# Performance work log

Hardware: AMD Instinct MI355X
Metric: run time of the kernel (lower is better)

The kernel has to match this reference:

```python
import jax, jax.numpy as jnp
import numpy as np

B, L1, L2 = 16, 32, 128
DEC = 512       # decoder_size
MEM = 512       # memory_bank_size
TOP = 50        # topic_num


def setup_inputs() -> dict:
    key = jax.random.key(0)
    ks = jax.random.split(key, 16)
    s = lambda fan_in: 1.0 / np.sqrt(fan_in)
    inp = {
        "decoder_state": jax.random.normal(ks[0], (B, DEC), jnp.float32),
        "doc_memory": jax.random.normal(ks[1], (B, L1, MEM), jnp.float32),
        "word_memory": jax.random.normal(ks[2], (B, L1, L2, MEM), jnp.float32),
        "topic_dist": jax.random.uniform(ks[3], (B, TOP), jnp.float32),
        "doc_mask": jnp.ones((B, L1), jnp.int32),
        "word_mask": jnp.ones((B, L1, L2), jnp.int32),
        # HierAttention params (PyTorch Linear weight layout: [out, in])
        "Wv": jax.random.uniform(ks[4], (1, DEC), jnp.float32, -s(DEC), s(DEC)),
        "Wd": jax.random.uniform(ks[5], (DEC, DEC), jnp.float32, -s(DEC), s(DEC)),
        "Wt": jax.random.uniform(ks[6], (DEC, TOP), jnp.float32, -s(TOP), s(TOP)),
        "Wm": jax.random.uniform(ks[7], (DEC, MEM), jnp.float32, -s(MEM), s(MEM)),
        # doc_attention (inner Attention) params
        "Wv2": jax.random.uniform(ks[8], (1, DEC), jnp.float32, -s(DEC), s(DEC)),
        "Wd2": jax.random.uniform(ks[9], (DEC, DEC), jnp.float32, -s(DEC), s(DEC)),
        "Wt2": jax.random.uniform(ks[10], (DEC, TOP), jnp.float32, -s(TOP), s(TOP)),
        "Wm2": jax.random.uniform(ks[11], (DEC, MEM), jnp.float32, -s(MEM), s(MEM)),
    }
    return inp


def reference(decoder_state, doc_memory, word_memory, topic_dist,
              doc_mask, word_mask,
              Wv, Wd, Wt, Wm, Wv2, Wd2, Wt2, Wm2):
    neg_inf = jnp.float32(-jnp.inf)

    # ---- word-level (HierAttention.score) ----
    enc_feat = jnp.einsum('bqwm,dm->bqwd', word_memory, Wm)      # [B,L1,L2,DEC]
    dec_feat = decoder_state @ Wd.T                              # [B,DEC]
    top_feat = topic_dist @ Wt.T                                 # [B,DEC]
    e = jnp.tanh(enc_feat + (dec_feat + top_feat)[:, None, None, :])
    word_scores = jnp.einsum('bqwd,od->bqw', e, Wv)[..., 0] if Wv.shape[0] != 1 else jnp.einsum('bqwd,d->bqw', e, Wv[0])
    word_scores = jnp.where(word_mask == 0, neg_inf, word_scores)
    word_attn = jax.nn.softmax(word_scores, axis=-1)             # [B,L1,L2]

    # ---- doc-level (Attention.score) ----
    enc_feat_d = jnp.einsum('bqm,dm->bqd', doc_memory, Wm2)      # [B,L1,DEC]
    dec_feat_d = decoder_state @ Wd2.T                           # [B,DEC]
    top_feat_d = topic_dist @ Wt2.T                              # [B,DEC]
    e_d = jnp.tanh(enc_feat_d + (dec_feat_d + top_feat_d)[:, None, :])
    doc_scores = jnp.einsum('bqd,d->bq', e_d, Wv2[0])            # [B,L1]
    doc_scores = jnp.where(doc_mask == 0, neg_inf, doc_scores)
    doc_attn = jax.nn.softmax(doc_scores, axis=-1)               # [B,L1]

    # ---- combine ----
    rescaled = doc_attn[..., None] * word_attn                   # [B,L1,L2]
    context = jnp.einsum('bqw,bqwm->bm', rescaled, word_memory)  # [B,MEM]
    return context, rescaled
```

## Files before the change

kernel.cpp:

```cpp
#include <hip/hip_runtime.h>
#include <hip/hip_bf16.h>
#include <math.h>

#define BATCH 16
#define L1 32
#define L2 128
#define DEC 512
#define MEM 512
#define TOPN 50
#define NROWS (BATCH * L1 * L2)
#define NBQ (BATCH * L1)

typedef short short8 __attribute__((ext_vector_type(8)));
typedef float f32x16 __attribute__((ext_vector_type(16)));

#define WS_WP     0
#define WS_WP2    131072
#define WS_BIAS1  262144
#define WS_BIAS2  270336
#define WS_DOCSC  278528

__device__ __forceinline__ unsigned int pkbf(float a, float b) {
    __hip_bfloat162 h = __float22bfloat162_rn(float2{a, b});
    union { __hip_bfloat162 h; unsigned int u; } c{h};
    return c.u;
}

__device__ __forceinline__ float fast_tanh(float x) {
    return 1.f - 2.f / (__expf(2.f * x) + 1.f);
}

__global__ __launch_bounds__(256) void setup_kernel(
    const float* __restrict__ Wm, const float* __restrict__ Wm2,
    unsigned short* __restrict__ Wp, unsigned short* __restrict__ Wp2,
    const float* __restrict__ dec, const float* __restrict__ topic,
    const float* __restrict__ Wd, const float* __restrict__ Wt,
    const float* __restrict__ Wd2, const float* __restrict__ Wt2,
    float* __restrict__ bias1, float* __restrict__ bias2,
    float* __restrict__ ctx_out)
{
    const int bid = blockIdx.x;
    const int tid = threadIdx.x;
    if (bid < 128) {
        int s = bid * 256 + tid;
        int C = s >> 10;
        int u = s & 1023;
        int nt = u >> 6, k8 = (u >> 5) & 1, n_in = u & 31;
        int d = nt * 32 + n_in;
        int k = C * 16 + k8 * 8;

        const float4* src = (const float4*)(Wm + (size_t)d * DEC + k);
        float4 v0 = src[0], v1 = src[1];
        uint4 v;
        v.x = pkbf(v0.x, v0.y); v.y = pkbf(v0.z, v0.w);
        v.z = pkbf(v1.x, v1.y); v.w = pkbf(v1.z, v1.w);
        ((uint4*)Wp)[s] = v;

        const float4* src2 = (const float4*)(Wm2 + (size_t)d * DEC + k);
        float4 w0 = src2[0], w1 = src2[1];
        uint4 w;
        w.x = pkbf(w0.x, w0.y); w.y = pkbf(w0.z, w0.w);
        w.z = pkbf(w1.x, w1.y); w.w = pkbf(w1.z, w1.w);
        ((uint4*)Wp2)[s] = w;
    } else if (bid < 128 + 4096) {
        int gw = (bid - 128) * 4 + (tid >> 6);
        int lane = tid & 63;
        int mat = gw >> 13;
        int rem = gw & 8191;
        int bb = rem >> 9;
        int d = rem & 511;

        const float* wrow = (mat ? Wd2 : Wd) + (size_t)d * DEC;
        const float* drow = dec + (size_t)bb * DEC;
        float4 a0 = ((const float4*)wrow)[lane * 2];
        float4 a1 = ((const float4*)wrow)[lane * 2 + 1];
        float4 x0 = ((const float4*)drow)[lane * 2];
        float4 x1 = ((const float4*)drow)[lane * 2 + 1];
        float acc = a0.x * x0.x;
        acc = fmaf(a0.y, x0.y, acc);
        acc = fmaf(a0.z, x0.z, acc);
        acc = fmaf(a0.w, x0.w, acc);
        acc = fmaf(a1.x, x1.x, acc);
        acc = fmaf(a1.y, x1.y, acc);
        acc = fmaf(a1.z, x1.z, acc);
        acc = fmaf(a1.w, x1.w, acc);
        const float* trow = (mat ? Wt2 : Wt) + (size_t)d * TOPN;
        if (lane < TOPN) acc = fmaf(trow[lane], topic[bb * TOPN + lane], acc);
#pragma unroll
        for (int o = 1; o <= 32; o <<= 1) acc += __shfl_xor(acc, o);
        if (lane == 0) (mat ? bias2 : bias1)[bb * DEC + d] = acc;
    } else {
        int i = (bid - (128 + 4096)) * 256 + tid;
        float4 z = {0.f, 0.f, 0.f, 0.f};
        ((float4*)ctx_out)[i * 2] = z;
        ((float4*)ctx_out)[i * 2 + 1] = z;
    }
}

__global__ __launch_bounds__(512, 2) void score_fused_kernel(
    const float* __restrict__ X,
    const unsigned short* __restrict__ Wp_,
    const float* __restrict__ Wv_,
    const float* __restrict__ bias_,
    const float* __restrict__ doc_scores,
    const int* __restrict__ doc_mask,
    const int* __restrict__ word_mask,
    float* __restrict__ rescaled_out,
    float* __restrict__ ctx_out,
    float* __restrict__ scores_out,
    int mode)
{
    __shared__ __align__(16) char lsA[128 * 1040];
    __shared__ float red[8][128];
    __shared__ float sS[128];
    __shared__ float rmax2[2], rsum2[2];
    __shared__ float s_dattn;
    __shared__ __align__(16) float4 part[3 * 128];

    const int tid = threadIdx.x;
    const int lane = tid & 63;
    const int w = tid >> 6;
    const int bid = blockIdx.x;
    const int r0 = bid * 128;
    const int col = lane & 31;
    const int h = lane >> 5;

    const int q0 = bid & 3;
    const int Q[4] = { q0, (q0 + 1) & 3, (q0 + 2) & 3, (q0 + 3) & 3 };
#define CH_AT(f) (Q[(f) >> 3] * 8 + ((f) & 7))

    const int scol = tid & 31;
    const int srow0 = tid >> 5;
    const float4* Xbase = (const float4*)X + (size_t)(r0 + srow0) * 128 + scol;
    char* const wbase = lsA + (size_t)srow0 * 1040 + scol * 8;

#define ISSUEQ(buf, qq) { _Pragma("unroll") for (int i = 0; i < 8; ++i) \
        buf[i] = Xbase[(size_t)(16 * i) * 128 + (qq) * 32]; }
#define WRITEQ(buf, qq) { _Pragma("unroll") for (int i = 0; i < 8; ++i) { \
        uint2 ww; ww.x = pkbf(buf[i].x, buf[i].y); ww.y = pkbf(buf[i].z, buf[i].w); \
        *(uint2*)(wbase + (size_t)(16 * i) * 1040 + (qq) * 256) = ww; } }
#define LGKMBAR { asm volatile("s_waitcnt lgkmcnt(0)" ::: "memory"); \
                  __builtin_amdgcn_s_barrier(); asm volatile("" ::: "memory"); }
#define MFMA(a, bb, c) __builtin_amdgcn_mfma_f32_32x32x16_bf16(a, bb, c, 0, 0, 0)

    const uint4* Bq4 = (const uint4*)Wp_;
    const int vB = w * 128 + lane;

    const char* const aR0 = lsA + (size_t)col * 1040 + h * 16;
    const char* const aR1 = aR0 + 32 * 1040;
    const char* const aR2 = aR0 + 64 * 1040;
    const char* const aR3 = aR0 + 96 * 1040;

    f32x16 acc[8];
#pragma unroll
    for (int t = 0; t < 8; ++t)
        acc[t] = (f32x16){0.f,0.f,0.f,0.f, 0.f,0.f,0.f,0.f, 0.f,0.f,0.f,0.f, 0.f,0.f,0.f,0.f};

    uint4 rb[4][2];

#define STEP(f, a0q, a1q, a2q, a3q) { \
        union { uint4 u; short8 s8; } b0{rb[(f) & 3][0]}, b1{rb[(f) & 3][1]}; \
        if ((f) + 4 < 32) { \
            const int cn_ = CH_AT((f) + 4); \
            rb[(f) & 3][0] = Bq4[(size_t)cn_ * 1024 + vB]; \
            rb[(f) & 3][1] = Bq4[(size_t)cn_ * 1024 + vB + 64]; \
        } \
        short8 a0 = *(const short8*)((a0q) + ((f) & 7) * 32); \
        short8 a1 = *(const short8*)((a1q) + ((f) & 7) * 32); \
        short8 a2 = *(const short8*)((a2q) + ((f) & 7) * 32); \
        short8 a3 = *(const short8*)((a3q) + ((f) & 7) * 32); \
        acc[0] = MFMA(a0, b0.s8, acc[0]); \
        acc[1] = MFMA(a0, b1.s8, acc[1]); \
        acc[2] = MFMA(a1, b0.s8, acc[2]); \
        acc[3] = MFMA(a1, b1.s8, acc[3]); \
        acc[4] = MFMA(a2, b0.s8, acc[4]); \
        acc[5] = MFMA(a2, b1.s8, acc[5]); \
        acc[6] = MFMA(a3, b0.s8, acc[6]); \
        acc[7] = MFMA(a3, b1.s8, acc[7]); }

#define QUARTER(j, f0) { \
        const int qo_ = Q[j] * 256; \
        const char* a0q = aR0 + qo_; const char* a1q = aR1 + qo_; \
        const char* a2q = aR2 + qo_; const char* a3q = aR3 + qo_; \
        STEP((f0) + 0, a0q, a1q, a2q, a3q) STEP((f0) + 1, a0q, a1q, a2q, a3q) \
        STEP((f0) + 2, a0q, a1q, a2q, a3q) STEP((f0) + 3, a0q, a1q, a2q, a3q) \
        STEP((f0) + 4, a0q, a1q, a2q, a3q) STEP((f0) + 5, a0q, a1q, a2q, a3q) \
        STEP((f0) + 6, a0q, a1q, a2q, a3q) STEP((f0) + 7, a0q, a1q, a2q, a3q) }

    float4 sb0[8], sb1[8];
    ISSUEQ(sb0, Q[0]);
    ISSUEQ(sb1, Q[1]);

    if (mode == 0 && tid < 32) {
        int b_ = bid >> 5;
        int di = b_ * 32 + tid;
        float dsv = doc_scores[di];
        if (doc_mask[di] == 0) dsv = -INFINITY;
        float mx = dsv;
#pragma unroll
        for (int o = 1; o <= 16; o <<= 1) mx = fmaxf(mx, __shfl_xor(mx, o));
        float e = __expf(dsv - mx);
        float sum = e;
#pragma unroll
        for (int o = 1; o <= 16; o <<= 1) sum += __shfl_xor(sum, o);
        if (tid == (bid & 31)) s_dattn = e / sum;
    }

    WRITEQ(sb0, Q[0]);
#pragma unroll
    for (int f = 0; f < 4; ++f) {
        const int c_ = CH_AT(f);
        rb[f][0] = Bq4[(size_t)c_ * 1024 + vB];
        rb[f][1] = Bq4[(size_t)c_ * 1024 + vB + 64];
    }
    LGKMBAR;

    ISSUEQ(sb0, Q[2]);
    QUARTER(0, 0);
    WRITEQ(sb1, Q[1]);
    LGKMBAR;

    ISSUEQ(sb1, Q[3]);
    QUARTER(1, 8);
    WRITEQ(sb0, Q[2]);
    LGKMBAR;

    QUARTER(2, 16);
    WRITEQ(sb1, Q[3]);
    LGKMBAR;

    QUARTER(3, 24);

    {
        const int d0 = w * 64 + col;
        const float wv0 = Wv_[d0], wv1 = Wv_[d0 + 32];
#pragma unroll
        for (int rg = 0; rg < 4; ++rg) {
            const int brg = mode ? (bid * 4 + rg) : (bid >> 5);
            const float bs0 = bias_[brg * DEC + d0];
            const float bs1 = bias_[brg * DEC + d0 + 32];
#pragma unroll
            for (int r = 0; r < 16; ++r) {
                float val = fmaf(wv0, fast_tanh(acc[rg * 2 + 0][r] + bs0),
                                 wv1 * fast_tanh(acc[rg * 2 + 1][r] + bs1));
                val += __shfl_xor(val, 16);
                val += __shfl_xor(val, 8);
                val += __shfl_xor(val, 4);
                val += __shfl_xor(val, 2);
                val += __shfl_xor(val, 1);
                if (col == r) {
                    int row_in = (r & 3) + 8 * (r >> 2) + 4 * h;
                    red[w][rg * 32 + row_in] = val;
                }
            }
        }
    }
    __syncthreads();

    if (mode) {
        if (tid < 128)
            scores_out[r0 + tid] = red[0][tid] + red[1][tid] + red[2][tid] + red[3][tid]
                                 + red[4][tid] + red[5][tid] + red[6][tid] + red[7][tid];
        return;
    }

    float e = 0.f, sv = 0.f;
    if (tid < 128) {
        sv = red[0][tid] + red[1][tid] + red[2][tid] + red[3][tid]
           + red[4][tid] + red[5][tid] + red[6][tid] + red[7][tid];
        if (word_mask[r0 + tid] == 0) sv = -INFINITY;
        float mx = sv;
#pragma unroll
        for (int o = 1; o <= 32; o <<= 1) mx = fmaxf(mx, __shfl_xor(mx, o));
        if (lane == 0) rmax2[w] = mx;
    }
    __syncthreads();
    if (tid < 128) {
        float mx = fmaxf(rmax2[0], rmax2[1]);
        e = __expf(sv - mx);
        float sum = e;
#pragma unroll
        for (int o = 1; o <= 32; o <<= 1) sum += __shfl_xor(sum, o);
        if (lane == 0) rsum2[w] = sum;
    }
    __syncthreads();
    if (tid < 128) {
        float sum = rsum2[0] + rsum2[1];
        float resc = s_dattn * (e / sum);
        sS[tid] = resc;
        rescaled_out[r0 + tid] = resc;
    }
    __syncthreads();

    const int b_ = bid >> 5;
    const int hh = tid >> 7;
    const int m4 = tid & 127;
    const float4* Xr = (const float4*)X + (size_t)r0 * 128 + (size_t)hh * 32 * 128 + m4;
    float4 a = {0.f, 0.f, 0.f, 0.f};
#pragma unroll 8
    for (int i = 0; i < 32; ++i) {
        float rr = sS[hh * 32 + i];
        float4 v = Xr[(size_t)i * 128];
        a.x = fmaf(rr, v.x, a.x);
        a.y = fmaf(rr, v.y, a.y);
        a.z = fmaf(rr, v.z, a.z);
        a.w = fmaf(rr, v.w, a.w);
    }
    if (hh) part[(hh - 1) * 128 + m4] = a;
    __syncthreads();
    if (hh == 0) {
        float4 p0 = part[m4], p1 = part[128 + m4], p2 = part[256 + m4];
        a.x += p0.x + p1.x + p2.x;
        a.y += p0.y + p1.y + p2.y;
        a.z += p0.z + p1.z + p2.z;
        a.w += p0.w + p1.w + p2.w;
        float* dst = ctx_out + (size_t)b_ * MEM + m4 * 4;
        atomicAdd(dst + 0, a.x);
        atomicAdd(dst + 1, a.y);
        atomicAdd(dst + 2, a.z);
        atomicAdd(dst + 3, a.w);
    }
}

extern "C" void kernel_launch(void* const* d_in, const int* in_sizes, int n_in,
                              void* d_out, int out_size, void* d_ws, size_t ws_size,
                              hipStream_t stream) {
    const float* decoder_state = (const float*)d_in[0];
    const float* doc_memory    = (const float*)d_in[1];
    const float* word_memory   = (const float*)d_in[2];
    const float* topic_dist    = (const float*)d_in[3];
    const int*   doc_mask      = (const int*)d_in[4];
    const int*   word_mask     = (const int*)d_in[5];
    const float* Wv  = (const float*)d_in[6];
    const float* Wd  = (const float*)d_in[7];
    const float* Wt  = (const float*)d_in[8];
    const float* Wm  = (const float*)d_in[9];
    const float* Wv2 = (const float*)d_in[10];
    const float* Wd2 = (const float*)d_in[11];
    const float* Wt2 = (const float*)d_in[12];
    const float* Wm2 = (const float*)d_in[13];

    float* ws = (float*)d_ws;
    unsigned short* Wp  = (unsigned short*)(ws + WS_WP);
    unsigned short* Wp2 = (unsigned short*)(ws + WS_WP2);
    float* bias1       = ws + WS_BIAS1;
    float* bias2       = ws + WS_BIAS2;
    float* doc_scores  = ws + WS_DOCSC;

    float* ctx_out      = (float*)d_out;
    float* rescaled_out = (float*)d_out + BATCH * MEM;

    setup_kernel<<<128 + 4096 + 4, 256, 0, stream>>>(Wm, Wm2, Wp, Wp2,
                                                     decoder_state, topic_dist,
                                                     Wd, Wt, Wd2, Wt2, bias1, bias2, ctx_out);
    score_fused_kernel<<<4, 512, 0, stream>>>(doc_memory, Wp2, Wv2, bias2,
                                              nullptr, nullptr, nullptr,
                                              nullptr, nullptr, doc_scores, 1);
    score_fused_kernel<<<NBQ, 512, 0, stream>>>(word_memory, Wp, Wv, bias1,
                                                doc_scores, doc_mask, word_mask,
                                                rescaled_out, ctx_out, nullptr, 0);
}
```

Measured before the change: 315.9 us.

## Split doc scoring into fp32 kernel and widen word kernel to 1024 threads

Replaces the 4-block MFMA doc-score launch with a dedicated 256-block fp32 dot-product kernel reading Wm2 directly, which removes the Wm2 bf16 packing from setup. The word kernel now runs 16 waves per block, each owning 32 output columns with one B fragment, and stages X in double-buffered quarter tiles (2x33KB) instead of one full 130KB tile. The goal is less LDS per block and more waves to hide latency. In exchange, each wave has less MFMA reuse per B load and there are more barriers and partial reductions.

```diff
diff --git a/kernel.cpp b/kernel.cpp
--- a/kernel.cpp
+++ b/kernel.cpp
@@ -30,9 +30,19 @@
     return 1.f - 2.f / (__expf(2.f * x) + 1.f);
 }
 
+__device__ __forceinline__ float wave_sum64(float v) {
+    v += __shfl_xor(v, 1);
+    v += __shfl_xor(v, 2);
+    v += __shfl_xor(v, 4);
+    v += __shfl_xor(v, 8);
+    v += __shfl_xor(v, 16);
+    v += __shfl_xor(v, 32);
+    return v;
+}
+
 __global__ __launch_bounds__(256) void setup_kernel(
-    const float* __restrict__ Wm, const float* __restrict__ Wm2,
-    unsigned short* __restrict__ Wp, unsigned short* __restrict__ Wp2,
+    const float* __restrict__ Wm,
+    unsigned short* __restrict__ Wp,
     const float* __restrict__ dec, const float* __restrict__ topic,
     const float* __restrict__ Wd, const float* __restrict__ Wt,
     const float* __restrict__ Wd2, const float* __restrict__ Wt2,
@@ -55,13 +65,6 @@
         v.x = pkbf(v0.x, v0.y); v.y = pkbf(v0.z, v0.w);
         v.z = pkbf(v1.x, v1.y); v.w = pkbf(v1.z, v1.w);
         ((uint4*)Wp)[s] = v;
-
-        const float4* src2 = (const float4*)(Wm2 + (size_t)d * DEC + k);
-        float4 w0 = src2[0], w1 = src2[1];
-        uint4 w;
-        w.x = pkbf(w0.x, w0.y); w.y = pkbf(w0.z, w0.w);
-        w.z = pkbf(w1.x, w1.y); w.w = pkbf(w1.z, w1.w);
-        ((uint4*)Wp2)[s] = w;
     } else if (bid < 128 + 4096) {
         int gw = (bid - 128) * 4 + (tid >> 6);
         int lane = tid & 63;
@@ -97,7 +100,73 @@
     }
 }
 
-__global__ __launch_bounds__(512, 2) void score_fused_kernel(
+__global__ __launch_bounds__(512) void doc_score_kernel(
+    const float* __restrict__ Xd,
+    const float* __restrict__ Wm2,
+    const float* __restrict__ Wv2,
+    const float* __restrict__ bias2,
+    float* __restrict__ doc_scores)
+{
+    __shared__ float wsum[2][8];
+    const int tid = threadIdx.x;
+    const int lane = tid & 63;
+    const int w = tid >> 6;
+    const int row0 = blockIdx.x * 2;
+    const int b = row0 >> 5;
+
+    const float4* X0 = (const float4*)(Xd + (size_t)row0 * MEM) + lane * 2;
+    const float4* X1 = (const float4*)(Xd + (size_t)(row0 + 1) * MEM) + lane * 2;
+    float4 xa0 = X0[0], xb0 = X0[1];
+    float4 xa1 = X1[0], xb1 = X1[1];
+
+    float s0 = 0.f, s1 = 0.f;
+#pragma unroll 2
+    for (int dd = 0; dd < 64; dd += 2) {
+        const int d = w * 64 + dd;
+        const float4* W0 = (const float4*)(Wm2 + (size_t)d * MEM) + lane * 2;
+        const float4* W1 = (const float4*)(Wm2 + (size_t)(d + 1) * MEM) + lane * 2;
+        float4 wa0 = W0[0], wb0 = W0[1];
+        float4 wa1 = W1[0], wb1 = W1[1];
+
+        float p00 = wa0.x * xa0.x, p01 = wa1.x * xa0.x;
+        float p10 = wa0.x * xa1.x, p11 = wa1.x * xa1.x;
+        p00 = fmaf(wa0.y, xa0.y, p00); p01 = fmaf(wa1.y, xa0.y, p01);
+        p10 = fmaf(wa0.y, xa1.y, p10); p11 = fmaf(wa1.y, xa1.y, p11);
+        p00 = fmaf(wa0.z, xa0.z, p00); p01 = fmaf(wa1.z, xa0.z, p01);
+        p10 = fmaf(wa0.z, xa1.z, p10); p11 = fmaf(wa1.z, xa1.z, p11);
+        p00 = fmaf(wa0.w, xa0.w, p00); p01 = fmaf(wa1.w, xa0.w, p01);
+        p10 = fmaf(wa0.w, xa1.w, p10); p11 = fmaf(wa1.w, xa1.w, p11);
+        p00 = fmaf(wb0.x, xb0.x, p00); p01 = fmaf(wb1.x, xb0.x, p01);
+        p10 = fmaf(wb0.x, xb1.x, p10); p11 = fmaf(wb1.x, xb1.x, p11);
+        p00 = fmaf(wb0.y, xb0.y, p00); p01 = fmaf(wb1.y, xb0.y, p01);
+        p10 = fmaf(wb0.y, xb1.y, p10); p11 = fmaf(wb1.y, xb1.y, p11);
+        p00 = fmaf(wb0.z, xb0.z, p00); p01 = fmaf(wb1.z, xb0.z, p01);
+        p10 = fmaf(wb0.z, xb1.z, p10); p11 = fmaf(wb1.z, xb1.z, p11);
+        p00 = fmaf(wb0.w, xb0.w, p00); p01 = fmaf(wb1.w, xb0.w, p01);
+        p10 = fmaf(wb0.w, xb1.w, p10); p11 = fmaf(wb1.w, xb1.w, p11);
+
+        p00 = wave_sum64(p00);
+        p01 = wave_sum64(p01);
+        p10 = wave_sum64(p10);
+        p11 = wave_sum64(p11);
+        if (lane == 0) {
+            float wva = Wv2[d], wvb = Wv2[d + 1];
+            float bsa = bias2[b * DEC + d], bsb = bias2[b * DEC + d + 1];
+            s0 += fmaf(wva, fast_tanh(p00 + bsa), wvb * fast_tanh(p01 + bsb));
+            s1 += fmaf(wva, fast_tanh(p10 + bsa), wvb * fast_tanh(p11 + bsb));
+        }
+    }
+    if (lane == 0) { wsum[0][w] = s0; wsum[1][w] = s1; }
+    __syncthreads();
+    if (tid < 2) {
+        float s = 0.f;
+#pragma unroll
+        for (int i = 0; i < 8; ++i) s += wsum[tid][i];
+        doc_scores[row0 + tid] = s;
+    }
+}
+
+__global__ __launch_bounds__(1024) void word_fused_kernel(
     const float* __restrict__ X,
     const unsigned short* __restrict__ Wp_,
     const float* __restrict__ Wv_,
@@ -106,16 +175,14 @@
     const int* __restrict__ doc_mask,
     const int* __restrict__ word_mask,
     float* __restrict__ rescaled_out,
-    float* __restrict__ ctx_out,
-    float* __restrict__ scores_out,
-    int mode)
+    float* __restrict__ ctx_out)
 {
-    __shared__ __align__(16) char lsA[128 * 1040];
-    __shared__ float red[8][128];
+    __shared__ __align__(16) char lsQ[2][128 * 264];
+    __shared__ float red[16][128];
     __shared__ float sS[128];
     __shared__ float rmax2[2], rsum2[2];
     __shared__ float s_dattn;
-    __shared__ __align__(16) float4 part[3 * 128];
+    __shared__ __align__(16) float4 part[7 * 128];
 
     const int tid = threadIdx.x;
     const int lane = tid & 63;
@@ -125,73 +192,49 @@
     const int col = lane & 31;
     const int h = lane >> 5;
 
-    const int q0 = bid & 3;
-    const int Q[4] = { q0, (q0 + 1) & 3, (q0 + 2) & 3, (q0 + 3) & 3 };
-#define CH_AT(f) (Q[(f) >> 3] * 8 + ((f) & 7))
-
     const int scol = tid & 31;
     const int srow0 = tid >> 5;
     const float4* Xbase = (const float4*)X + (size_t)(r0 + srow0) * 128 + scol;
-    char* const wbase = lsA + (size_t)srow0 * 1040 + scol * 8;
-
-#define ISSUEQ(buf, qq) { _Pragma("unroll") for (int i = 0; i < 8; ++i) \
-        buf[i] = Xbase[(size_t)(16 * i) * 128 + (qq) * 32]; }
-#define WRITEQ(buf, qq) { _Pragma("unroll") for (int i = 0; i < 8; ++i) { \
-        uint2 ww; ww.x = pkbf(buf[i].x, buf[i].y); ww.y = pkbf(buf[i].z, buf[i].w); \
-        *(uint2*)(wbase + (size_t)(16 * i) * 1040 + (qq) * 256) = ww; } }
+
+    float4 sb[4];
+#define ISSUEQ(qq) { _Pragma("unroll") for (int i = 0; i < 4; ++i) \
+        sb[i] = Xbase[(size_t)(32 * i) * 128 + (qq) * 32]; }
+#define WRITEQ(pb) { char* wp = lsQ[pb] + (size_t)srow0 * 264 + scol * 8; \
+    _Pragma("unroll") for (int i = 0; i < 4; ++i) { \
+        uint2 ww; ww.x = pkbf(sb[i].x, sb[i].y); ww.y = pkbf(sb[i].z, sb[i].w); \
+        *(uint2*)(wp + (size_t)(32 * i) * 264) = ww; } }
 #define LGKMBAR { asm volatile("s_waitcnt lgkmcnt(0)" ::: "memory"); \
                   __builtin_amdgcn_s_barrier(); asm volatile("" ::: "memory"); }
 #define MFMA(a, bb, c) __builtin_amdgcn_mfma_f32_32x32x16_bf16(a, bb, c, 0, 0, 0)
 
     const uint4* Bq4 = (const uint4*)Wp_;
-    const int vB = w * 128 + lane;
-
-    const char* const aR0 = lsA + (size_t)col * 1040 + h * 16;
-    const char* const aR1 = aR0 + 32 * 1040;
-    const char* const aR2 = aR0 + 64 * 1040;
-    const char* const aR3 = aR0 + 96 * 1040;
-
-    f32x16 acc[8];
-#pragma unroll
-    for (int t = 0; t < 8; ++t)
-        acc[t] = (f32x16){0.f,0.f,0.f,0.f, 0.f,0.f,0.f,0.f, 0.f,0.f,0.f,0.f, 0.f,0.f,0.f,0.f};
-
-    uint4 rb[4][2];
-
-#define STEP(f, a0q, a1q, a2q, a3q) { \
-        union { uint4 u; short8 s8; } b0{rb[(f) & 3][0]}, b1{rb[(f) & 3][1]}; \
-        if ((f) + 4 < 32) { \
-            const int cn_ = CH_AT((f) + 4); \
-            rb[(f) & 3][0] = Bq4[(size_t)cn_ * 1024 + vB]; \
-            rb[(f) & 3][1] = Bq4[(size_t)cn_ * 1024 + vB + 64]; \
-        } \
-        short8 a0 = *(const short8*)((a0q) + ((f) & 7) * 32); \
-        short8 a1 = *(const short8*)((a1q) + ((f) & 7) * 32); \
-        short8 a2 = *(const short8*)((a2q) + ((f) & 7) * 32); \
-        short8 a3 = *(const short8*)((a3q) + ((f) & 7) * 32); \
-        acc[0] = MFMA(a0, b0.s8, acc[0]); \
-        acc[1] = MFMA(a0, b1.s8, acc[1]); \
-        acc[2] = MFMA(a1, b0.s8, acc[2]); \
-        acc[3] = MFMA(a1, b1.s8, acc[3]); \
-        acc[4] = MFMA(a2, b0.s8, acc[4]); \
-        acc[5] = MFMA(a2, b1.s8, acc[5]); \
-        acc[6] = MFMA(a3, b0.s8, acc[6]); \
-        acc[7] = MFMA(a3, b1.s8, acc[7]); }
-
-#define QUARTER(j, f0) { \
-        const int qo_ = Q[j] * 256; \
-        const char* a0q = aR0 + qo_; const char* a1q = aR1 + qo_; \
-        const char* a2q = aR2 + qo_; const char* a3q = aR3 + qo_; \
-        STEP((f0) + 0, a0q, a1q, a2q, a3q) STEP((f0) + 1, a0q, a1q, a2q, a3q) \
-        STEP((f0) + 2, a0q, a1q, a2q, a3q) STEP((f0) + 3, a0q, a1q, a2q, a3q) \
-        STEP((f0) + 4, a0q, a1q, a2q, a3q) STEP((f0) + 5, a0q, a1q, a2q, a3q) \
-        STEP((f0) + 6, a0q, a1q, a2q, a3q) STEP((f0) + 7, a0q, a1q, a2q, a3q) }
-
-    float4 sb0[8], sb1[8];
-    ISSUEQ(sb0, Q[0]);
-    ISSUEQ(sb1, Q[1]);
-
-    if (mode == 0 && tid < 32) {
+    const int vB = w * 64 + lane;
+
+    f32x16 acc0, acc1, acc2, acc3;
+    acc0 = acc1 = acc2 = acc3 =
+        (f32x16){0.f,0.f,0.f,0.f, 0.f,0.f,0.f,0.f, 0.f,0.f,0.f,0.f, 0.f,0.f,0.f,0.f};
+
+    uint4 rb[4];
+
+#define STEP(f, pb) { \
+        union { uint4 u; short8 s8; } bb{rb[(f) & 3]}; \
+        if ((f) + 4 < 32) rb[(f) & 3] = Bq4[(size_t)((f) + 4) * 1024 + vB]; \
+        const char* ab = lsQ[pb] + (size_t)col * 264 + h * 16 + ((f) & 7) * 32; \
+        short8 a0 = *(const short8*)(ab); \
+        short8 a1 = *(const short8*)(ab + 32 * 264); \
+        short8 a2 = *(const short8*)(ab + 64 * 264); \
+        short8 a3 = *(const short8*)(ab + 96 * 264); \
+        acc0 = MFMA(a0, bb.s8, acc0); \
+        acc1 = MFMA(a1, bb.s8, acc1); \
+        acc2 = MFMA(a2, bb.s8, acc2); \
+        acc3 = MFMA(a3, bb.s8, acc3); }
+
+#define QUARTER(f0, pb) { STEP((f0)+0, pb) STEP((f0)+1, pb) STEP((f0)+2, pb) STEP((f0)+3, pb) \
+                          STEP((f0)+4, pb) STEP((f0)+5, pb) STEP((f0)+6, pb) STEP((f0)+7, pb) }
+
+    ISSUEQ(0);
+
+    if (tid < 32) {
         int b_ = bid >> 5;
         int di = b_ * 32 + tid;
         float dsv = doc_scores[di];
@@ -206,73 +249,54 @@
         if (tid == (bid & 31)) s_dattn = e / sum;
     }
 
-    WRITEQ(sb0, Q[0]);
-#pragma unroll
-    for (int f = 0; f < 4; ++f) {
-        const int c_ = CH_AT(f);
-        rb[f][0] = Bq4[(size_t)c_ * 1024 + vB];
-        rb[f][1] = Bq4[(size_t)c_ * 1024 + vB + 64];
-    }
+    WRITEQ(0);
+#pragma unroll
+    for (int f = 0; f < 4; ++f) rb[f] = Bq4[(size_t)f * 1024 + vB];
     LGKMBAR;
 
-    ISSUEQ(sb0, Q[2]);
+    ISSUEQ(1);
     QUARTER(0, 0);
-    WRITEQ(sb1, Q[1]);
+    WRITEQ(1);
     LGKMBAR;
 
-    ISSUEQ(sb1, Q[3]);
-    QUARTER(1, 8);
-    WRITEQ(sb0, Q[2]);
+    ISSUEQ(2);
+    QUARTER(8, 1);
+    WRITEQ(0);
     LGKMBAR;
 
-    QUARTER(2, 16);
-    WRITEQ(sb1, Q[3]);
+    ISSUEQ(3);
+    QUARTER(16, 0);
+    WRITEQ(1);
     LGKMBAR;
 
-    QUARTER(3, 24);
+    QUARTER(24, 1);
 
     {
-        const int d0 = w * 64 + col;
-        const float wv0 = Wv_[d0], wv1 = Wv_[d0 + 32];
-#pragma unroll
-        for (int rg = 0; rg < 4; ++rg) {
-            const int brg = mode ? (bid * 4 + rg) : (bid >> 5);
-            const float bs0 = bias_[brg * DEC + d0];
-            const float bs1 = bias_[brg * DEC + d0 + 32];
-#pragma unroll
-            for (int r = 0; r < 16; ++r) {
-                float val = fmaf(wv0, fast_tanh(acc[rg * 2 + 0][r] + bs0),
-                                 wv1 * fast_tanh(acc[rg * 2 + 1][r] + bs1));
-                val += __shfl_xor(val, 16);
-                val += __shfl_xor(val, 8);
-                val += __shfl_xor(val, 4);
-                val += __shfl_xor(val, 2);
-                val += __shfl_xor(val, 1);
-                if (col == r) {
-                    int row_in = (r & 3) + 8 * (r >> 2) + 4 * h;
-                    red[w][rg * 32 + row_in] = val;
-                }
-            }
-        }
-    }
-    __syncthreads();
-
-    if (mode) {
-        if (tid < 128)
-            scores_out[r0 + tid] = red[0][tid] + red[1][tid] + red[2][tid] + red[3][tid]
-                                 + red[4][tid] + red[5][tid] + red[6][tid] + red[7][tid];
-        return;
-    }
+        const int d0 = w * 32 + col;
+        const float wv0 = Wv_[d0];
+        const int bb_ = bid >> 5;
+        const float bs0 = bias_[bb_ * DEC + d0];
+#define EPI(rg, accN) { _Pragma("unroll") for (int r = 0; r < 16; ++r) { \
+            float val = wv0 * fast_tanh(accN[r] + bs0); \
+            val += __shfl_xor(val, 16); val += __shfl_xor(val, 8); \
+            val += __shfl_xor(val, 4);  val += __shfl_xor(val, 2); \
+            val += __shfl_xor(val, 1); \
+            if (col == r) red[w][(rg) * 32 + ((r & 3) + 8 * (r >> 2) + 4 * h)] = val; } }
+        EPI(0, acc0) EPI(1, acc1) EPI(2, acc2) EPI(3, acc3)
+#undef EPI
+    }
+    __syncthreads();
 
     float e = 0.f, sv = 0.f;
     if (tid < 128) {
-        sv = red[0][tid] + red[1][tid] + red[2][tid] + red[3][tid]
-           + red[4][tid] + red[5][tid] + red[6][tid] + red[7][tid];
+        sv = 0.f;
+#pragma unroll
+        for (int i = 0; i < 16; ++i) sv += red[i][tid];
         if (word_mask[r0 + tid] == 0) sv = -INFINITY;
         float mx = sv;
 #pragma unroll
         for (int o = 1; o <= 32; o <<= 1) mx = fmaxf(mx, __shfl_xor(mx, o));
-        if (lane == 0) rmax2[w] = mx;
+        if (lane == 0) rmax2[tid >> 6] = mx;
     }
     __syncthreads();
     if (tid < 128) {
@@ -281,7 +305,7 @@
         float sum = e;
 #pragma unroll
         for (int o = 1; o <= 32; o <<= 1) sum += __shfl_xor(sum, o);
-        if (lane == 0) rsum2[w] = sum;
+        if (lane == 0) rsum2[tid >> 6] = sum;
     }
     __syncthreads();
     if (tid < 128) {
@@ -295,11 +319,11 @@
     const int b_ = bid >> 5;
     const int hh = tid >> 7;
     const int m4 = tid & 127;
-    const float4* Xr = (const float4*)X + (size_t)r0 * 128 + (size_t)hh * 32 * 128 + m4;
+    const float4* Xr = (const float4*)X + (size_t)(r0 + hh * 16) * 128 + m4;
     float4 a = {0.f, 0.f, 0.f, 0.f};
-#pragma unroll 8
-    for (int i = 0; i < 32; ++i) {
-        float rr = sS[hh * 32 + i];
+#pragma unroll 4
+    for (int i = 0; i < 16; ++i) {
+        float rr = sS[hh * 16 + i];
         float4 v = Xr[(size_t)i * 128];
         a.x = fmaf(rr, v.x, a.x);
         a.y = fmaf(rr, v.y, a.y);
@@ -309,11 +333,11 @@
     if (hh) part[(hh - 1) * 128 + m4] = a;
     __syncthreads();
     if (hh == 0) {
-        float4 p0 = part[m4], p1 = part[128 + m4], p2 = part[256 + m4];
-        a.x += p0.x + p1.x + p2.x;
-        a.y += p0.y + p1.y + p2.y;
-        a.z += p0.z + p1.z + p2.z;
-        a.w += p0.w + p1.w + p2.w;
+#pragma unroll
+        for (int p = 0; p < 7; ++p) {
+            float4 pp = part[p * 128 + m4];
+            a.x += pp.x; a.y += pp.y; a.z += pp.z; a.w += pp.w;
+        }
         float* dst = ctx_out + (size_t)b_ * MEM + m4 * 4;
         atomicAdd(dst + 0, a.x);
         atomicAdd(dst + 1, a.y);
@@ -342,7 +366,6 @@
 
     float* ws = (float*)d_ws;
     unsigned short* Wp  = (unsigned short*)(ws + WS_WP);
-    unsigned short* Wp2 = (unsigned short*)(ws + WS_WP2);
     float* bias1       = ws + WS_BIAS1;
     float* bias2       = ws + WS_BIAS2;
     float* doc_scores  = ws + WS_DOCSC;
@@ -350,13 +373,11 @@
     float* ctx_out      = (float*)d_out;
     float* rescaled_out = (float*)d_out + BATCH * MEM;
 
-    setup_kernel<<<128 + 4096 + 4, 256, 0, stream>>>(Wm, Wm2, Wp, Wp2,
+    setup_kernel<<<128 + 4096 + 4, 256, 0, stream>>>(Wm, Wp,
                                                      decoder_state, topic_dist,
                                                      Wd, Wt, Wd2, Wt2, bias1, bias2, ctx_out);
-    score_fused_kernel<<<4, 512, 0, stream>>>(doc_memory, Wp2, Wv2, bias2,
-                                              nullptr, nullptr, nullptr,
-                                              nullptr, nullptr, doc_scores, 1);
-    score_fused_kernel<<<NBQ, 512, 0, stream>>>(word_memory, Wp, Wv, bias1,
+    doc_score_kernel<<<256, 512, 0, stream>>>(doc_memory, Wm2, Wv2, bias2, doc_scores);
+    word_fused_kernel<<<NBQ, 1024, 0, stream>>>(word_memory, Wp, Wv, bias1,
                                                 doc_scores, doc_mask, word_mask,
-                                                rescaled_out, ctx_out, nullptr, 0);
-}
+                                                rescaled_out, ctx_out);
+}
```

Measured after the change: 429.2 us. 35.9% more time.
